# Kernel tuning notes

Hardware: AMD Instinct MI355X
Metric: run time of the kernel (lower is better)

## Reference

```python
import jax, jax.numpy as jnp
import numpy as np

B, S, E, H, V, C = 512, 64, 512, 1024, 1024, 1000
PAD = 0

def setup_inputs() -> dict:
    key = jax.random.key(0)
    ks = jax.random.split(key, 10)
    x_in = jax.random.randint(ks[0], (B, S), 0, V)
    x_lengths = jax.random.randint(ks[1], (B,), 1, S + 1)
    emb_w = jax.random.normal(ks[2], (V, E), jnp.float32) * 0.02
    emb_w = emb_w.at[PAD].set(0.0)  # padding_idx row is zero
    s_h = 1.0 / np.sqrt(H)
    w_ih = jax.random.uniform(ks[3], (H, E), jnp.float32, -s_h, s_h)
    b_ih = jax.random.uniform(ks[4], (H,), jnp.float32, -s_h, s_h)
    w_hh = jax.random.uniform(ks[5], (H, H), jnp.float32, -s_h, s_h)
    b_hh = jax.random.uniform(ks[6], (H,), jnp.float32, -s_h, s_h)
    fc1_w = jax.random.uniform(ks[7], (H, H), jnp.float32, -s_h, s_h)
    fc1_b = jnp.zeros((H,), jnp.float32)
    fc2_w = jax.random.uniform(ks[8], (C, H), jnp.float32, -s_h, s_h)
    fc2_b = jnp.zeros((C,), jnp.float32)
    return dict(x_in=x_in, x_lengths=x_lengths, emb_w=emb_w, w_ih=w_ih, b_ih=b_ih,
                w_hh=w_hh, b_hh=b_hh, fc1_w=fc1_w, fc1_b=fc1_b, fc2_w=fc2_w, fc2_b=fc2_b)

def reference(x_in, x_lengths, emb_w, w_ih, b_ih, w_hh, b_hh, fc1_w, fc1_b, fc2_w, fc2_b):
    # Embedding lookup: [B,S,E]
    x_emb = emb_w[x_in]
    # Precompute input projections for all steps: [S,B,H]
    x_proj = jnp.einsum('bse,he->sbh', x_emb, w_ih) + b_ih
    def step(h, xp):
        h_new = jnp.tanh(xp + h @ w_hh.T + b_hh)
        return h_new, h_new
    h0 = jnp.zeros((x_in.shape[0], w_hh.shape[0]), x_proj.dtype)
    _, hs = jax.lax.scan(step, h0, x_proj)          # [S,B,H]
    y_out = jnp.transpose(hs, (1, 0, 2))            # [B,S,H]
    # column_gather: final valid hidden per sequence
    idx = (x_lengths - 1).astype(jnp.int32)
    y_last = jnp.take_along_axis(y_out, idx[:, None, None], axis=1)[:, 0, :]  # [B,H]
    # dropout in eval mode = identity
    y = jax.nn.relu(y_last @ fc1_w.T + fc1_b)
    y = y @ fc2_w.T + fc2_b
    return y
```

## Files before the change

kernel.cpp:

```cpp
#include <hip/hip_runtime.h>
#include <hip/hip_bf16.h>
#include <stdint.h>
#include <stddef.h>

#define B_SZ 512
#define S_SZ 64
#define E_SZ 512
#define H_SZ 1024
#define V_SZ 1024
#define C_SZ 1000

typedef __hip_bfloat16 bf16;
typedef __attribute__((ext_vector_type(8))) __bf16 bf16x8;
typedef __attribute__((ext_vector_type(4))) float f32x4;

#define EMB_OFF   (0ull)
#define WIH_OFF   (1ull << 20)
#define WHH_OFF   (2ull << 20)
#define FC1_OFF   (4ull << 20)
#define FC2_OFF   (6ull << 20)
#define HB_OFF    (8ull << 20)
#define XP_OFF    (12ull << 20)
#define BAR_OFF   (FC2_OFF + 2048000ull)

__device__ __forceinline__ void gl_lds16(const void* g, void* l) {
  __builtin_amdgcn_global_load_lds(
      (const __attribute__((address_space(1))) unsigned int*)g,
      (__attribute__((address_space(3))) unsigned int*)l, 16, 0, 0);
}

__global__ __launch_bounds__(256) void prep_kernel(
    const float* __restrict__ emb_w, const float* __restrict__ w_ih,
    const float* __restrict__ w_hh, const float* __restrict__ fc1_w,
    const float* __restrict__ fc2_w, char* __restrict__ ws) {
  bf16* emb = (bf16*)(ws + EMB_OFF);
  bf16* wih = (bf16*)(ws + WIH_OFF);
  bf16* whh = (bf16*)(ws + WHH_OFF);
  bf16* fc1 = (bf16*)(ws + FC1_OFF);
  bf16* fc2 = (bf16*)(ws + FC2_OFF);
  bf16* h0  = (bf16*)(ws + HB_OFF);

  const long N_EMB = 524288, N_WIH = 524288, N_WHH = 1048576;
  const long N_FC1 = 1048576, N_FC2 = 1048576, N_H0 = 524288;
  const long TOTAL = N_EMB + N_WIH + N_WHH + N_FC1 + N_FC2 + N_H0;

  long stride = (long)gridDim.x * blockDim.x;
  for (long i = (long)blockIdx.x * blockDim.x + threadIdx.x; i < TOTAL; i += stride) {
    long j = i;
    if (j < N_EMB) {
      emb[j] = (j < E_SZ) ? __float2bfloat16(0.f) : __float2bfloat16(emb_w[j]);
      continue;
    }
    j -= N_EMB;
    if (j < N_WIH) { wih[j] = __float2bfloat16(w_ih[j]); continue; }
    j -= N_WIH;
    if (j < N_WHH) { whh[j] = __float2bfloat16(w_hh[j]); continue; }
    j -= N_WHH;
    if (j < N_FC1) { fc1[j] = __float2bfloat16(fc1_w[j]); continue; }
    j -= N_FC1;
    if (j < N_FC2) {
      fc2[j] = (j < (long)C_SZ * H_SZ) ? __float2bfloat16(fc2_w[j]) : __float2bfloat16(0.f);
      continue;
    }
    j -= N_FC2;
    h0[j] = __float2bfloat16(0.f);
  }
}

__global__ __launch_bounds__(256) void xproj_kernel(
    const int* __restrict__ x_in, const float* __restrict__ b_ih,
    char* __restrict__ ws) {
  const bf16* emb = (const bf16*)(ws + EMB_OFF);
  const bf16* wih = (const bf16*)(ws + WIH_OFF);
  bf16* xp = (bf16*)(ws + XP_OFF);

  __shared__ bf16 Asm[2][128][64];
  __shared__ bf16 Bsm[2][128][64];

  const int tid = threadIdx.x;
  const int lane = tid & 63;
  const int wid = tid >> 6;
  const int mb = blockIdx.x >> 3;
  const int nb = blockIdx.x & 7;
  const int rowBase = mb * 128;
  const int colBase = nb * 128;
  const int s = rowBase >> 9;

  const int lrow = lane >> 3;
  const int lchk = lane & 7;

  int tok[4];
#pragma unroll
  for (int i = 0; i < 4; ++i) {
    int rt = wid * 32 + i * 8 + lrow;
    int b = (rowBase + rt) & 511;
    tok[i] = x_in[b * S_SZ + s];
  }

  const int wr = wid >> 1, wc = wid & 1;
  f32x4 acc[4][4];
#pragma unroll
  for (int i = 0; i < 4; ++i)
#pragma unroll
    for (int j = 0; j < 4; ++j) acc[i][j] = (f32x4){0.f, 0.f, 0.f, 0.f};

  auto stage = [&](int buf, int k0) {
#pragma unroll
    for (int i = 0; i < 4; ++i) {
      int rt = wid * 32 + i * 8;
      int sc = (lchk ^ ((rt + lrow) & 7)) * 8;
      gl_lds16(emb + (size_t)tok[i] * E_SZ + k0 + sc, &Asm[buf][rt][0]);
    }
#pragma unroll
    for (int i = 0; i < 4; ++i) {
      int rt = wid * 32 + i * 8;
      int sc = (lchk ^ ((rt + lrow) & 7)) * 8;
      gl_lds16(wih + (size_t)(colBase + rt + lrow) * E_SZ + k0 + sc, &Bsm[buf][rt][0]);
    }
  };

  stage(0, 0);
  __syncthreads();
  int cur = 0;
  for (int t8 = 0; t8 < 8; ++t8) {
    if (t8 < 7) stage(cur ^ 1, (t8 + 1) * 64);
#pragma unroll
    for (int kk = 0; kk < 2; ++kk) {
      const int kfc = kk * 4 + (lane >> 4);
      bf16x8 a[4], b[4];
#pragma unroll
      for (int i = 0; i < 4; ++i) {
        int r = wr * 64 + i * 16 + (lane & 15);
        a[i] = *(const bf16x8*)&Asm[cur][r][(kfc ^ (r & 7)) * 8];
      }
#pragma unroll
      for (int j = 0; j < 4; ++j) {
        int r = wc * 64 + j * 16 + (lane & 15);
        b[j] = *(const bf16x8*)&Bsm[cur][r][(kfc ^ (r & 7)) * 8];
      }
#pragma unroll
      for (int i = 0; i < 4; ++i)
#pragma unroll
        for (int j = 0; j < 4; ++j)
          acc[i][j] = __builtin_amdgcn_mfma_f32_16x16x32_bf16(a[i], b[j], acc[i][j], 0, 0, 0);
    }
    __syncthreads();
    cur ^= 1;
  }

  const int crow = (lane >> 4) * 4;
  const int ccol = lane & 15;
#pragma unroll
  for (int j = 0; j < 4; ++j) {
    const int col = colBase + wc * 64 + j * 16 + ccol;
    const float bias = b_ih[col];
#pragma unroll
    for (int i = 0; i < 4; ++i) {
      const int r0 = rowBase + wr * 64 + i * 16 + crow;
#pragma unroll
      for (int reg = 0; reg < 4; ++reg) {
        float v = acc[i][j][reg] + bias;
        xp[(size_t)(r0 + reg) * H_SZ + col] = __float2bfloat16(v);
      }
    }
  }
}

__device__ __forceinline__ void stage_rowsA(const bf16* src, bf16* ApBuf,
                                            int lane, int wid, int rowBase, int k0) {
  const int r = lane >> 3, c = lane & 7;
  const bf16* g = src + (size_t)(rowBase + wid * 8 + r) * H_SZ + k0 + ((c ^ r) << 3);
  gl_lds16(g, ApBuf + wid * 512);
}

__device__ __forceinline__ void stage_pinB(const bf16* w, bf16* Bsm,
                                           int lane, int wid, int colBase) {
#pragma unroll
  for (int oo = 0; oo < 32; ++oo) {
    const int o = wid * 32 + oo;
    const int r = o >> 1, hf = o & 1;
    const bf16* g = w + (size_t)(colBase + r) * H_SZ + hf * 512 + ((lane ^ (r & 7)) << 3);
    gl_lds16(g, Bsm + r * H_SZ + hf * 512);
  }
}

__device__ __forceinline__ void clusterbar(unsigned* bar, unsigned target, bool acq) {
  __syncthreads();
  if (threadIdx.x == 0) {
    __hip_atomic_fetch_add(bar, 1u, __ATOMIC_RELEASE, __HIP_MEMORY_SCOPE_AGENT);
    while (__hip_atomic_load(bar, __ATOMIC_RELAXED, __HIP_MEMORY_SCOPE_AGENT) < target)
      __builtin_amdgcn_s_sleep(1);
    if (acq)
      (void)__hip_atomic_load(bar, __ATOMIC_ACQUIRE, __HIP_MEMORY_SCOPE_AGENT);
  }
  asm volatile("" ::: "memory");
  __syncthreads();
}

template <int MODE>
__device__ __forceinline__ void phase(
    const bf16* __restrict__ Asrc, const bf16* Bsm, bf16* Ap,
    int lane, int wid, int rowBase, int colBase,
    const float* __restrict__ bias, const bf16* __restrict__ xpt,
    const int* __restrict__ lens, int t,
    bf16* __restrict__ dst_bf, bf16* __restrict__ yl,
    float* __restrict__ outf) {
  const int wr = wid >> 1, wc = wid & 1;
  const int r0 = rowBase + wr * 16 + (lane >> 4) * 4;
  const int c0 = colBase + wc * 32 + (lane & 15);
  const int sw = lane & 7;

  f32x4 acc[2];
  acc[0] = (f32x4){0.f, 0.f, 0.f, 0.f};
  acc[1] = (f32x4){0.f, 0.f, 0.f, 0.f};

  bf16 xv[2][4];
  if constexpr (MODE == 0) {
#pragma unroll
    for (int j = 0; j < 2; ++j)
#pragma unroll
      for (int reg = 0; reg < 4; ++reg)
        xv[j][reg] = xpt[(size_t)(r0 + reg) * H_SZ + c0 + j * 16];
  }

  stage_rowsA(Asrc, Ap + 0 * 2048, lane, wid, rowBase, 0);
  asm volatile("" ::: "memory");
  stage_rowsA(Asrc, Ap + 1 * 2048, lane, wid, rowBase, 64);
  asm volatile("" ::: "memory");
  stage_rowsA(Asrc, Ap + 2 * 2048, lane, wid, rowBase, 128);

#pragma unroll
  for (int i = 0; i < 16; ++i) {
    if (i < 14)       asm volatile("s_waitcnt vmcnt(2)" ::: "memory");
    else if (i == 14) asm volatile("s_waitcnt vmcnt(1)" ::: "memory");
    else              asm volatile("s_waitcnt vmcnt(0)" ::: "memory");
    __builtin_amdgcn_s_barrier();
    asm volatile("" ::: "memory");
    if (i < 13)
      stage_rowsA(Asrc, Ap + ((i + 3) & 3) * 2048, lane, wid, rowBase, (i + 3) * 64);
    const bf16* Ab = Ap + (i & 3) * 2048;
#pragma unroll
    for (int kk = 0; kk < 2; ++kk) {
      const int kfc = kk * 4 + (lane >> 4);
      const int ra = wr * 16 + (lane & 15);
      bf16x8 a = *(const bf16x8*)(Ab + ra * 64 + ((kfc ^ sw) << 3));
      const int rb0 = wc * 32 + (lane & 15);
      bf16x8 b0 = *(const bf16x8*)(Bsm + rb0 * H_SZ + ((i * 8 + (kfc ^ sw)) << 3));
      bf16x8 b1 = *(const bf16x8*)(Bsm + (rb0 + 16) * H_SZ + ((i * 8 + (kfc ^ sw)) << 3));
      acc[0] = __builtin_amdgcn_mfma_f32_16x16x32_bf16(a, b0, acc[0], 0, 0, 0);
      acc[1] = __builtin_amdgcn_mfma_f32_16x16x32_bf16(a, b1, acc[1], 0, 0, 0);
    }
  }

#pragma unroll
  for (int j = 0; j < 2; ++j) {
    const int col = c0 + j * 16;
#pragma unroll
    for (int reg = 0; reg < 4; ++reg) {
      const int row = r0 + reg;
      float v = acc[j][reg];
      if constexpr (MODE == 0) {
        v += bias[col] + __bfloat162float(xv[j][reg]);
        v = fminf(fmaxf(v, -15.f), 15.f);
        float e = __expf(2.f * v);
        float h = (e - 1.f) / (e + 1.f);
        bf16 hb = __float2bfloat16(h);
        dst_bf[(size_t)row * H_SZ + col] = hb;
        if (t == lens[row] - 1) yl[(size_t)row * H_SZ + col] = hb;
      } else if constexpr (MODE == 1) {
        v += bias[col];
        dst_bf[(size_t)row * H_SZ + col] = __float2bfloat16(fmaxf(v, 0.f));
      } else {
        if (col < C_SZ) outf[(size_t)row * C_SZ + col] = v + bias[col];
      }
    }
  }
}

__global__ __launch_bounds__(256) void rnn_fused_kernel(
    const float* __restrict__ b_hh, const float* __restrict__ fc1_b,
    const float* __restrict__ fc2_b, const int* __restrict__ lens,
    char* __restrict__ ws, float* __restrict__ out) {
  extern __shared__ char smem[];
  bf16* Bsm = (bf16*)smem;
  bf16* Ap  = (bf16*)(smem + 131072);

  const int tid = threadIdx.x;
  const int lane = tid & 63, wid = tid >> 6;
  const int bid = blockIdx.x;
  const int mb = ((bid & 7) << 1) | ((bid >> 3) & 1);
  const int nb = bid >> 4;
  const int rowBase = mb * 32, colBase = nb * 64;

  const bf16* whh  = (const bf16*)(ws + WHH_OFF);
  const bf16* fc1w = (const bf16*)(ws + FC1_OFF);
  const bf16* fc2w = (const bf16*)(ws + FC2_OFF);
  const bf16* xp   = (const bf16*)(ws + XP_OFF);
  bf16* hb = (bf16*)(ws + HB_OFF);
  bf16* yl = (bf16*)(ws + EMB_OFF);
  bf16* y1 = (bf16*)(ws + WIH_OFF);
  unsigned* bar = (unsigned*)(ws + BAR_OFF + (size_t)mb * 128);

  stage_pinB(whh, Bsm, lane, wid, colBase);
  asm volatile("s_waitcnt vmcnt(0)" ::: "memory");
  __builtin_amdgcn_s_barrier();
  asm volatile("" ::: "memory");

  unsigned ep = 0;
#pragma unroll 1
  for (int t = 0; t < S_SZ; ++t) {
    const bf16* hsrc = hb + ((size_t)(t & 3) << 19);
    bf16* hdst = hb + ((size_t)((t + 1) & 3) << 19);
    phase<0>(hsrc, Bsm, Ap, lane, wid, rowBase, colBase, b_hh,
             xp + (size_t)t * (B_SZ * H_SZ), lens, t, hdst, yl, nullptr);
    ++ep;
    clusterbar(bar, ep * 16u, (t & 3) == 3);
  }

  stage_pinB(fc1w, Bsm, lane, wid, colBase);
  asm volatile("s_waitcnt vmcnt(0)" ::: "memory");
  __builtin_amdgcn_s_barrier();
  asm volatile("" ::: "memory");
  phase<1>(yl, Bsm, Ap, lane, wid, rowBase, colBase, fc1_b,
           nullptr, nullptr, 0, y1, nullptr, nullptr);
  ++ep;
  clusterbar(bar, ep * 16u, true);

  stage_pinB(fc2w, Bsm, lane, wid, colBase);
  asm volatile("s_waitcnt vmcnt(0)" ::: "memory");
  __builtin_amdgcn_s_barrier();
  asm volatile("" ::: "memory");
  phase<2>(y1, Bsm, Ap, lane, wid, rowBase, colBase, fc2_b,
           nullptr, nullptr, 0, nullptr, nullptr, out);
}

extern "C" void kernel_launch(void* const* d_in, const int* in_sizes, int n_in,
                              void* d_out, int out_size, void* d_ws, size_t ws_size,
                              hipStream_t stream) {
  (void)in_sizes; (void)n_in; (void)out_size; (void)ws_size;
  const int* x_in = (const int*)d_in[0];
  const int* x_len = (const int*)d_in[1];
  const float* emb_w = (const float*)d_in[2];
  const float* w_ih = (const float*)d_in[3];
  const float* b_ih = (const float*)d_in[4];
  const float* w_hh = (const float*)d_in[5];
  const float* b_hh = (const float*)d_in[6];
  const float* fc1_w = (const float*)d_in[7];
  const float* fc1_b = (const float*)d_in[8];
  const float* fc2_w = (const float*)d_in[9];
  const float* fc2_b = (const float*)d_in[10];
  char* ws = (char*)d_ws;
  float* out = (float*)d_out;

  prep_kernel<<<2048, 256, 0, stream>>>(emb_w, w_ih, w_hh, fc1_w, fc2_w, ws);

  xproj_kernel<<<2048, 256, 0, stream>>>(x_in, b_ih, ws);

  (void)hipFuncSetAttribute((const void*)rnn_fused_kernel,
                            hipFuncAttributeMaxDynamicSharedMemorySize, 147456);
  rnn_fused_kernel<<<256, 256, 147456, stream>>>(b_hh, fc1_b, fc2_b, x_len, ws, out);
}
```

Measured before the change: 737.5 us.

## Hold recurrent weights in registers across 512-thread blocks instead of LDS

Each block now runs 8 waves; each wave owns a 16x16 output tile and keeps its full K=1024 slice of the weight matrix in VGPRs (32 bf16x8 vectors) rather than pinning a 128KB weight tile in shared memory. This removes the per-step LDS reads of B and shrinks shared memory to a small A staging buffer. The next step's x-projection values and the lengths are also prefetched into registers ahead of time. The cost is heavy register pressure (128 VGPRs just for weights) and an uneven A staging path where only 4 of the 8 waves issue loads.

```diff
diff --git a/kernel.cpp b/kernel.cpp
--- a/kernel.cpp
+++ b/kernel.cpp
@@ -166,24 +166,6 @@
   }
 }
 
-__device__ __forceinline__ void stage_rowsA(const bf16* src, bf16* ApBuf,
-                                            int lane, int wid, int rowBase, int k0) {
-  const int r = lane >> 3, c = lane & 7;
-  const bf16* g = src + (size_t)(rowBase + wid * 8 + r) * H_SZ + k0 + ((c ^ r) << 3);
-  gl_lds16(g, ApBuf + wid * 512);
-}
-
-__device__ __forceinline__ void stage_pinB(const bf16* w, bf16* Bsm,
-                                           int lane, int wid, int colBase) {
-#pragma unroll
-  for (int oo = 0; oo < 32; ++oo) {
-    const int o = wid * 32 + oo;
-    const int r = o >> 1, hf = o & 1;
-    const bf16* g = w + (size_t)(colBase + r) * H_SZ + hf * 512 + ((lane ^ (r & 7)) << 3);
-    gl_lds16(g, Bsm + r * H_SZ + hf * 512);
-  }
-}
-
 __device__ __forceinline__ void clusterbar(unsigned* bar, unsigned target, bool acq) {
   __syncthreads();
   if (threadIdx.x == 0) {
@@ -197,100 +179,92 @@
   __syncthreads();
 }
 
+__device__ __forceinline__ void load_breg(bf16x8 (&breg)[16][2],
+                                          const bf16* w, int c0, int lane) {
+  const bf16* wrow = w + (size_t)c0 * H_SZ + ((lane >> 4) << 3);
+#pragma unroll
+  for (int i = 0; i < 16; ++i)
+#pragma unroll
+    for (int kk = 0; kk < 2; ++kk)
+      breg[i][kk] = *(const bf16x8*)(wrow + i * 64 + kk * 32);
+}
+
 template <int MODE>
 __device__ __forceinline__ void phase(
-    const bf16* __restrict__ Asrc, const bf16* Bsm, bf16* Ap,
-    int lane, int wid, int rowBase, int colBase,
-    const float* __restrict__ bias, const bf16* __restrict__ xpt,
-    const int* __restrict__ lens, int t,
-    bf16* __restrict__ dst_bf, bf16* __restrict__ yl,
-    float* __restrict__ outf) {
-  const int wr = wid >> 1, wc = wid & 1;
-  const int r0 = rowBase + wr * 16 + (lane >> 4) * 4;
-  const int c0 = colBase + wc * 32 + (lane & 15);
-  const int sw = lane & 7;
-
-  f32x4 acc[2];
-  acc[0] = (f32x4){0.f, 0.f, 0.f, 0.f};
-  acc[1] = (f32x4){0.f, 0.f, 0.f, 0.f};
-
-  bf16 xv[2][4];
-  if constexpr (MODE == 0) {
-#pragma unroll
-    for (int j = 0; j < 2; ++j)
-#pragma unroll
-      for (int reg = 0; reg < 4; ++reg)
-        xv[j][reg] = xpt[(size_t)(r0 + reg) * H_SZ + c0 + j * 16];
-  }
-
-  stage_rowsA(Asrc, Ap + 0 * 2048, lane, wid, rowBase, 0);
-  asm volatile("" ::: "memory");
-  stage_rowsA(Asrc, Ap + 1 * 2048, lane, wid, rowBase, 64);
-  asm volatile("" ::: "memory");
-  stage_rowsA(Asrc, Ap + 2 * 2048, lane, wid, rowBase, 128);
+    const bf16* __restrict__ Asrc, const bf16x8 (&breg)[16][2], bf16* Ap,
+    int lane, int wid, int rowBase, float bias_v,
+    const bf16 (&xv)[4], const int (&lenv)[4], int t, int r0, int c0,
+    bf16* __restrict__ dst, bf16* __restrict__ yl, float* __restrict__ outf) {
+  const int wr = wid & 1;
+  f32x4 acc = (f32x4){0.f, 0.f, 0.f, 0.f};
+
+  const bf16* sbase = Asrc +
+      (size_t)(rowBase + (wid & 1) * 16 + (lane & 15)) * H_SZ +
+      (wid >> 1) * 32 + ((lane >> 4) << 3);
+  bf16* sdst0 = Ap + ((wid & 1) * 2 + (wid >> 1)) * 512;
+
+  if (wid < 4) {
+    gl_lds16(sbase, sdst0);
+    asm volatile("" ::: "memory");
+    gl_lds16(sbase + 64, sdst0 + 2048);
+    asm volatile("" ::: "memory");
+    gl_lds16(sbase + 128, sdst0 + 2 * 2048);
+  }
 
 #pragma unroll
   for (int i = 0; i < 16; ++i) {
-    if (i < 14)       asm volatile("s_waitcnt vmcnt(2)" ::: "memory");
-    else if (i == 14) asm volatile("s_waitcnt vmcnt(1)" ::: "memory");
-    else              asm volatile("s_waitcnt vmcnt(0)" ::: "memory");
+    if (wid < 4) {
+      if (i < 14)       asm volatile("s_waitcnt vmcnt(2)" ::: "memory");
+      else if (i == 14) asm volatile("s_waitcnt vmcnt(1)" ::: "memory");
+      else              asm volatile("s_waitcnt vmcnt(0)" ::: "memory");
+    }
     __builtin_amdgcn_s_barrier();
     asm volatile("" ::: "memory");
-    if (i < 13)
-      stage_rowsA(Asrc, Ap + ((i + 3) & 3) * 2048, lane, wid, rowBase, (i + 3) * 64);
-    const bf16* Ab = Ap + (i & 3) * 2048;
-#pragma unroll
-    for (int kk = 0; kk < 2; ++kk) {
-      const int kfc = kk * 4 + (lane >> 4);
-      const int ra = wr * 16 + (lane & 15);
-      bf16x8 a = *(const bf16x8*)(Ab + ra * 64 + ((kfc ^ sw) << 3));
-      const int rb0 = wc * 32 + (lane & 15);
-      bf16x8 b0 = *(const bf16x8*)(Bsm + rb0 * H_SZ + ((i * 8 + (kfc ^ sw)) << 3));
-      bf16x8 b1 = *(const bf16x8*)(Bsm + (rb0 + 16) * H_SZ + ((i * 8 + (kfc ^ sw)) << 3));
-      acc[0] = __builtin_amdgcn_mfma_f32_16x16x32_bf16(a, b0, acc[0], 0, 0, 0);
-      acc[1] = __builtin_amdgcn_mfma_f32_16x16x32_bf16(a, b1, acc[1], 0, 0, 0);
-    }
-  }
-
-#pragma unroll
-  for (int j = 0; j < 2; ++j) {
-    const int col = c0 + j * 16;
-#pragma unroll
-    for (int reg = 0; reg < 4; ++reg) {
-      const int row = r0 + reg;
-      float v = acc[j][reg];
-      if constexpr (MODE == 0) {
-        v += bias[col] + __bfloat162float(xv[j][reg]);
-        v = fminf(fmaxf(v, -15.f), 15.f);
-        float e = __expf(2.f * v);
-        float h = (e - 1.f) / (e + 1.f);
-        bf16 hb = __float2bfloat16(h);
-        dst_bf[(size_t)row * H_SZ + col] = hb;
-        if (t == lens[row] - 1) yl[(size_t)row * H_SZ + col] = hb;
-      } else if constexpr (MODE == 1) {
-        v += bias[col];
-        dst_bf[(size_t)row * H_SZ + col] = __float2bfloat16(fmaxf(v, 0.f));
-      } else {
-        if (col < C_SZ) outf[(size_t)row * C_SZ + col] = v + bias[col];
-      }
-    }
-  }
-}
-
-__global__ __launch_bounds__(256) void rnn_fused_kernel(
+    if (wid < 4 && i < 13)
+      gl_lds16(sbase + (i + 3) * 64, sdst0 + ((i + 3) & 3) * 2048);
+    const bf16* Ab = Ap + (i & 3) * 2048 + wr * 1024 + lane * 8;
+    bf16x8 a0 = *(const bf16x8*)(Ab);
+    bf16x8 a1 = *(const bf16x8*)(Ab + 512);
+    acc = __builtin_amdgcn_mfma_f32_16x16x32_bf16(a0, breg[i][0], acc, 0, 0, 0);
+    acc = __builtin_amdgcn_mfma_f32_16x16x32_bf16(a1, breg[i][1], acc, 0, 0, 0);
+  }
+
+#pragma unroll
+  for (int reg = 0; reg < 4; ++reg) {
+    const int row = r0 + reg;
+    float v = acc[reg];
+    if constexpr (MODE == 0) {
+      v += bias_v + __bfloat162float(xv[reg]);
+      v = fminf(fmaxf(v, -15.f), 15.f);
+      float e = __expf(2.f * v);
+      float h = (e - 1.f) / (e + 1.f);
+      bf16 hb = __float2bfloat16(h);
+      dst[(size_t)row * H_SZ + c0] = hb;
+      if (t == lenv[reg] - 1) yl[(size_t)row * H_SZ + c0] = hb;
+    } else if constexpr (MODE == 1) {
+      dst[(size_t)row * H_SZ + c0] = __float2bfloat16(fmaxf(v + bias_v, 0.f));
+    } else {
+      if (c0 < C_SZ) outf[(size_t)row * C_SZ + c0] = v + bias_v;
+    }
+  }
+}
+
+__global__ __launch_bounds__(512, 2) void rnn_fused_kernel(
     const float* __restrict__ b_hh, const float* __restrict__ fc1_b,
     const float* __restrict__ fc2_b, const int* __restrict__ lens,
     char* __restrict__ ws, float* __restrict__ out) {
-  extern __shared__ char smem[];
-  bf16* Bsm = (bf16*)smem;
-  bf16* Ap  = (bf16*)(smem + 131072);
+  __shared__ bf16 Ap[8192];
 
   const int tid = threadIdx.x;
   const int lane = tid & 63, wid = tid >> 6;
   const int bid = blockIdx.x;
   const int mb = ((bid & 7) << 1) | ((bid >> 3) & 1);
   const int nb = bid >> 4;
-  const int rowBase = mb * 32, colBase = nb * 64;
+  const int rowBase = mb * 32;
+  const int colBase = nb * 64;
+  const int wr = wid & 1, wc = wid >> 1;
+  const int r0 = rowBase + wr * 16 + ((lane >> 4) << 2);
+  const int c0 = colBase + wc * 16 + (lane & 15);
 
   const bf16* whh  = (const bf16*)(ws + WHH_OFF);
   const bf16* fc1w = (const bf16*)(ws + FC1_OFF);
@@ -301,37 +275,43 @@
   bf16* y1 = (bf16*)(ws + WIH_OFF);
   unsigned* bar = (unsigned*)(ws + BAR_OFF + (size_t)mb * 128);
 
-  stage_pinB(whh, Bsm, lane, wid, colBase);
-  asm volatile("s_waitcnt vmcnt(0)" ::: "memory");
-  __builtin_amdgcn_s_barrier();
-  asm volatile("" ::: "memory");
-
-  unsigned ep = 0;
+  const float bhv = b_hh[c0];
+  int lenv[4];
+#pragma unroll
+  for (int reg = 0; reg < 4; ++reg) lenv[reg] = lens[r0 + reg];
+
+  bf16x8 breg[16][2];
+  load_breg(breg, whh, c0, lane);
+
+  bf16 xv[4];
+#pragma unroll
+  for (int reg = 0; reg < 4; ++reg) xv[reg] = xp[(size_t)(r0 + reg) * H_SZ + c0];
+
 #pragma unroll 1
   for (int t = 0; t < S_SZ; ++t) {
     const bf16* hsrc = hb + ((size_t)(t & 3) << 19);
     bf16* hdst = hb + ((size_t)((t + 1) & 3) << 19);
-    phase<0>(hsrc, Bsm, Ap, lane, wid, rowBase, colBase, b_hh,
-             xp + (size_t)t * (B_SZ * H_SZ), lens, t, hdst, yl, nullptr);
-    ++ep;
-    clusterbar(bar, ep * 16u, (t & 3) == 3);
-  }
-
-  stage_pinB(fc1w, Bsm, lane, wid, colBase);
-  asm volatile("s_waitcnt vmcnt(0)" ::: "memory");
-  __builtin_amdgcn_s_barrier();
-  asm volatile("" ::: "memory");
-  phase<1>(yl, Bsm, Ap, lane, wid, rowBase, colBase, fc1_b,
-           nullptr, nullptr, 0, y1, nullptr, nullptr);
-  ++ep;
-  clusterbar(bar, ep * 16u, true);
-
-  stage_pinB(fc2w, Bsm, lane, wid, colBase);
-  asm volatile("s_waitcnt vmcnt(0)" ::: "memory");
-  __builtin_amdgcn_s_barrier();
-  asm volatile("" ::: "memory");
-  phase<2>(y1, Bsm, Ap, lane, wid, rowBase, colBase, fc2_b,
-           nullptr, nullptr, 0, nullptr, nullptr, out);
+    phase<0>(hsrc, breg, Ap, lane, wid, rowBase, bhv, xv, lenv, t, r0, c0,
+             hdst, yl, nullptr);
+    if (t < S_SZ - 1) {
+      const bf16* xpn = xp + (size_t)(t + 1) * (B_SZ * H_SZ);
+#pragma unroll
+      for (int reg = 0; reg < 4; ++reg)
+        xv[reg] = xpn[(size_t)(r0 + reg) * H_SZ + c0];
+    }
+    clusterbar(bar, (unsigned)(t + 1) * 16u, (t & 3) == 3);
+  }
+
+  load_breg(breg, fc1w, c0, lane);
+  const float b1v = fc1_b[c0];
+  phase<1>(yl, breg, Ap, lane, wid, rowBase, b1v, xv, lenv, 0, r0, c0,
+           y1, nullptr, nullptr);
+  clusterbar(bar, 65u * 16u, true);
+
+  load_breg(breg, fc2w, c0, lane);
+  const float b2v = (c0 < C_SZ) ? fc2_b[c0] : 0.f;
+  phase<2>(y1, breg, Ap, lane, wid, rowBase, b2v, xv, lenv, 0, r0, c0,
+           nullptr, nullptr, out);
 }
 
 extern "C" void kernel_launch(void* const* d_in, const int* in_sizes, int n_in,
@@ -356,7 +336,5 @@
 
   xproj_kernel<<<2048, 256, 0, stream>>>(x_in, b_ih, ws);
 
-  (void)hipFuncSetAttribute((const void*)rnn_fused_kernel,
-                            hipFuncAttributeMaxDynamicSharedMemorySize, 147456);
-  rnn_fused_kernel<<<256, 256, 147456, stream>>>(b_hh, fc1_b, fc2_b, x_len, ws, out);
-}
+  rnn_fused_kernel<<<256, 512, 0, stream>>>(b_hh, fc1_b, fc2_b, x_len, ws, out);
+}
```

Measured after the change: 629.7 us. 14.6% less time.
